# Kernel tuning notes

Measured on AMD Instinct MI355X. Metric: run time of the kernel, lower is better.

The kernel has to match this reference:

```python
import jax, jax.numpy as jnp
import numpy as np

B, T, D_IN, D, N = 8, 1024, 512, 512, 64

def setup_inputs() -> dict:
    key = jax.random.key(0)
    ks = jax.random.split(key, 8)
    s = 0.02  # weight init scale keeps tanh/softmax in sane range
    return {
        'x': jax.random.normal(ks[0], (B, T, D_IN), jnp.float32),
        'h_tape_init': jax.random.normal(ks[1], (B, N, D), jnp.float32),
        'h_work_init': jax.random.normal(ks[2], (B, D), jnp.float32) * 0.1,
        'W_h': jax.random.normal(ks[3], (D, D), jnp.float32) * s,
        'W_xz': jax.random.normal(ks[4], (2 * D, D_IN), jnp.float32) * s,
        'b_h': jnp.zeros((D,), jnp.float32),
        'W_write': jax.random.normal(ks[5], (D, D), jnp.float32) * s,
        'g_z': jnp.ones((D,), jnp.float32),
        'g_r': jnp.ones((D,), jnp.float32),
        'g_h': jnp.ones((D,), jnp.float32),
        'b_gate': jnp.zeros((D,), jnp.float32),
    }

def reference(x, h_tape_init, h_work_init, W_h, W_xz, b_h, W_write, g_z, g_r, g_h, b_gate):
    d = W_h.shape[0]
    scale = 1.0 / np.sqrt(d).astype(np.float32)
    xz = jnp.einsum('btk,ek->bte', x, W_xz)          # [B,T,2D]
    x_proj = xz[..., :d]
    z = xz[..., d:]

    def step(carry, inp):
        h_tape, h_work = carry                        # [B,N,D], [B,D]
        x_t, z_t = inp                                # [B,D], [B,D]
        read_scores = jnp.einsum('bd,bnd->bn', h_work, h_tape) * scale
        read_attn = jax.nn.softmax(read_scores, axis=-1)
        read_val = jnp.einsum('bn,bnd->bd', read_attn, h_tape)
        h_new = jnp.tanh(x_t + h_work @ W_h.T + read_val + b_h)
        write_val = h_new @ W_write.T
        write_scores = jnp.einsum('bd,bnd->bn', write_val, h_tape) * scale
        write_attn = jax.nn.softmax(write_scores, axis=-1)[..., None]  # [B,N,1]
        h_tape_new = h_tape * (1.0 - write_attn) + write_val[:, None, :] * write_attn
        gate_in = jnp.clip(z_t * g_z + read_val * g_r + h_new * g_h + b_gate, -20.0, 20.0)
        out = h_new * jax.nn.silu(gate_in)
        return (h_tape_new, h_new), out

    (h_tape_final, _), outs = jax.lax.scan(
        step, (h_tape_init, h_work_init),
        (jnp.swapaxes(x_proj, 0, 1), jnp.swapaxes(z, 0, 1)))
    return jnp.swapaxes(outs, 0, 1), h_tape_final
```

## Files before the change

### kernel.cpp

```cpp
#include <hip/hip_runtime.h>
#include <math.h>

#define BB 8
#define TT 1024
#define DD 512
#define NT 64
#define NSL 8
#define DSL 64
#define PITCH 68

static __device__ __forceinline__ float aload(const float* p) {
    return __hip_atomic_load(p, __ATOMIC_RELAXED, __HIP_MEMORY_SCOPE_AGENT);
}
static __device__ __forceinline__ void astore(float* p, float v) {
    __hip_atomic_store(p, v, __ATOMIC_RELAXED, __HIP_MEMORY_SCOPE_AGENT);
}

static __device__ __forceinline__ float redux8(float v) {
    v += __shfl_xor(v, 1);
    v += __shfl_xor(v, 2);
    v += __shfl_xor(v, 4);
    return v;
}

static __device__ __forceinline__ float softmax64(float sc) {
    float m = sc;
    #pragma unroll
    for (int off = 32; off > 0; off >>= 1) m = fmaxf(m, __shfl_xor(m, off));
    float e = __expf(sc - m);
    float s = e;
    #pragma unroll
    for (int off = 32; off > 0; off >>= 1) s += __shfl_xor(s, off);
    return e / s;
}

static __device__ __forceinline__ float dot64(const float4 (&w)[16], const float* hr) {
    float a0 = 0.f, a1 = 0.f, a2 = 0.f, a3 = 0.f;
    #pragma unroll
    for (int j = 0; j < 16; j += 4) {
        float4 h0 = *(const float4*)(hr + 4 * (j + 0));
        float4 h1 = *(const float4*)(hr + 4 * (j + 1));
        float4 h2 = *(const float4*)(hr + 4 * (j + 2));
        float4 h3 = *(const float4*)(hr + 4 * (j + 3));
        a0 += w[j + 0].x * h0.x + w[j + 0].y * h0.y + w[j + 0].z * h0.z + w[j + 0].w * h0.w;
        a1 += w[j + 1].x * h1.x + w[j + 1].y * h1.y + w[j + 1].z * h1.z + w[j + 1].w * h1.w;
        a2 += w[j + 2].x * h2.x + w[j + 2].y * h2.y + w[j + 2].z * h2.z + w[j + 2].w * h2.w;
        a3 += w[j + 3].x * h3.x + w[j + 3].y * h3.y + w[j + 3].z * h3.z + w[j + 3].w * h3.w;
    }
    return (a0 + a1) + (a2 + a3);
}

__global__ __launch_bounds__(256) void proj_kernel(const float* __restrict__ x,
                                                   const float* __restrict__ Wxz,
                                                   float* __restrict__ xp,
                                                   float* __restrict__ z) {
    __shared__ float As[16][66];
    __shared__ float Bs[16][66];
    const int m0 = blockIdx.x * 64;
    const int n0 = blockIdx.y * 64;
    const int tid = threadIdx.x;
    const int tm = tid / 16, tn = tid % 16;
    float c[4][4] = {};
    for (int k0 = 0; k0 < 512; k0 += 16) {
        const int r = tid >> 2, c4 = (tid & 3) * 4;
        float4 a4 = *(const float4*)(x + (size_t)(m0 + r) * 512 + k0 + c4);
        float4 b4 = *(const float4*)(Wxz + (size_t)(n0 + r) * 512 + k0 + c4);
        As[c4 + 0][r] = a4.x; As[c4 + 1][r] = a4.y; As[c4 + 2][r] = a4.z; As[c4 + 3][r] = a4.w;
        Bs[c4 + 0][r] = b4.x; Bs[c4 + 1][r] = b4.y; Bs[c4 + 2][r] = b4.z; Bs[c4 + 3][r] = b4.w;
        __syncthreads();
        #pragma unroll
        for (int k = 0; k < 16; ++k) {
            float a0 = As[k][tm * 4 + 0], a1 = As[k][tm * 4 + 1];
            float a2 = As[k][tm * 4 + 2], a3 = As[k][tm * 4 + 3];
            float b0 = Bs[k][tn * 4 + 0], b1 = Bs[k][tn * 4 + 1];
            float b2 = Bs[k][tn * 4 + 2], b3 = Bs[k][tn * 4 + 3];
            c[0][0] += a0 * b0; c[0][1] += a0 * b1; c[0][2] += a0 * b2; c[0][3] += a0 * b3;
            c[1][0] += a1 * b0; c[1][1] += a1 * b1; c[1][2] += a1 * b2; c[1][3] += a1 * b3;
            c[2][0] += a2 * b0; c[2][1] += a2 * b1; c[2][2] += a2 * b2; c[2][3] += a2 * b3;
            c[3][0] += a3 * b0; c[3][1] += a3 * b1; c[3][2] += a3 * b2; c[3][3] += a3 * b3;
        }
        __syncthreads();
    }
    #pragma unroll
    for (int i = 0; i < 4; ++i) {
        const int m = m0 + tm * 4 + i;
        #pragma unroll
        for (int j = 0; j < 4; ++j) {
            const int e = n0 + tn * 4 + j;
            if (e < 512) xp[(size_t)m * 512 + e] = c[i][j];
            else         z[(size_t)m * 512 + (e - 512)] = c[i][j];
        }
    }
}

__global__ __launch_bounds__(512, 2) void rec_kernel(
    const float* __restrict__ tape0, const float* __restrict__ hwork0,
    const float* __restrict__ W_h, const float* __restrict__ b_h,
    const float* __restrict__ W_write,
    const float* __restrict__ g_z, const float* __restrict__ g_r,
    const float* __restrict__ g_h, const float* __restrict__ b_gate,
    const float* __restrict__ Zbuf,
    float* __restrict__ out, float* __restrict__ tape_out,
    float* g_hn, float* g_pws, float* g_ps0, float* g_phwv,
    unsigned* flags) {
    const int b = blockIdx.x & 7;
    const int s = blockIdx.x >> 3;
    const int tid = threadIdx.x;
    const int row = tid >> 3;
    const int l = tid & 7;
    const int d0 = s * DSL;
    const int drow = d0 + row;
    const float scale = 0.044194173824159216f;

    __shared__ __attribute__((aligned(16))) float tape[NT][PITCH];
    __shared__ __attribute__((aligned(16))) float hw2[8][PITCH];
    __shared__ __attribute__((aligned(16))) float red[8][PITCH];
    __shared__ __attribute__((aligned(16))) float hn_s[DSL];
    __shared__ __attribute__((aligned(16))) float wv_s[DSL];
    __shared__ __attribute__((aligned(16))) float a_l[NT];
    __shared__ __attribute__((aligned(16))) float r_l[NT];
    __shared__ __attribute__((aligned(16))) float rv[DSL];
    __shared__ __attribute__((aligned(16))) float xp_s[DSL];
    __shared__ __attribute__((aligned(16))) float z_s[DSL];

    unsigned* flagA = flags + b * 128;
    unsigned* flagB = flags + b * 128 + 64;

    float4 wh[16], ww[16];
    {
        const float4* w1 = (const float4*)(W_h + (size_t)drow * DD + l * 64);
        const float4* w2 = (const float4*)(W_write + (size_t)drow * DD + l * 64);
        #pragma unroll
        for (int j = 0; j < 16; ++j) wh[j] = w1[j];
        #pragma unroll
        for (int j = 0; j < 16; ++j) ww[j] = w2[j];
    }
    const float bh_r = b_h[drow];
    const int de = (tid >= 64 && tid < 128) ? (tid - 64) : 0;
    const float gzr = g_z[d0 + de], grr = g_r[d0 + de], ghr = g_h[d0 + de], bgr = b_gate[d0 + de];

    {
        const float4* tsrc = (const float4*)(tape0 + ((size_t)(b * NT + row)) * DD + d0 + l * 8);
        float4 t0 = tsrc[0], t1 = tsrc[1];
        *(float4*)&tape[row][l * 8] = t0;
        *(float4*)&tape[row][l * 8 + 4] = t1;
    }
    if (tid < 128) {
        float4 h4 = *(const float4*)(hwork0 + (size_t)b * DD + tid * 4);
        const int e = tid * 4;
        *(float4*)&hw2[e >> 6][e & 63] = h4;
    }
    __syncthreads();

    {
        float acc = 0.f;
        #pragma unroll
        for (int i = 0; i < 8; ++i) {
            const int dl = l * 8 + i;
            const int e = d0 + dl;
            acc += hw2[e >> 6][e & 63] * tape[row][dl];
        }
        acc = redux8(acc);
        if (l == 0) astore(&g_ps0[(b * NSL + s) * NT + row], acc);
    }
    __syncthreads();
    if (tid == 0) {
        __builtin_amdgcn_s_waitcnt(0);
        __hip_atomic_fetch_add(flagB, 1u, __ATOMIC_RELAXED, __HIP_MEMORY_SCOPE_AGENT);
        while (__hip_atomic_load(flagB, __ATOMIC_RELAXED, __HIP_MEMORY_SCOPE_AGENT) < 8u) {}
    }
    __syncthreads();
    if (tid < 64) {
        float s0 = 0.f;
        #pragma unroll
        for (int ss = 0; ss < 8; ++ss) s0 += aload(&g_ps0[(b * NSL + ss) * NT + tid]);
        r_l[tid] = softmax64(s0 * scale);
    }
    __syncthreads();
    {
        const int nc = tid >> 6, d = tid & 63;
        float acc = 0.f;
        #pragma unroll
        for (int i = 0; i < 8; ++i) acc += r_l[nc * 8 + i] * tape[nc * 8 + i][d];
        red[nc][d] = acc;
    }
    __syncthreads();
    if (tid < 64) {
        float acc = 0.f;
        #pragma unroll
        for (int nc = 0; nc < 8; ++nc) acc += red[nc][tid];
        rv[tid] = acc;
    }
    if (tid >= 64 && tid < 128) {
        xp_s[tid - 64] = out[((size_t)(b * TT)) * DD + d0 + (tid - 64)];
    } else if (tid >= 128 && tid < 192) {
        z_s[tid - 128] = Zbuf[((size_t)(b * TT)) * DD + d0 + (tid - 128)];
    }
    __syncthreads();

    for (int t = 0; t < TT; ++t) {
        {
            float acc = dot64(wh, &hw2[l][0]);
            acc = redux8(acc);
            float hn = tanhf(acc + xp_s[row] + rv[row] + bh_r);
            if (l == 0) hn_s[row] = hn;
        }
        __syncthreads();
        if (tid < 64) {
            astore(&g_hn[b * DD + d0 + tid], hn_s[tid]);
        } else if (tid < 128) {
            const int d = tid - 64;
            const float h = hn_s[d];
            float g = z_s[d] * gzr + rv[d] * grr + h * ghr + bgr;
            g = fminf(fmaxf(g, -20.f), 20.f);
            const float sig = 1.f / (1.f + __expf(-g));
            out[((size_t)(b * TT + t)) * DD + d0 + d] = h * g * sig;
        }
        __syncthreads();
        if (tid == 0) {
            __builtin_amdgcn_s_waitcnt(0);
            __hip_atomic_fetch_add(flagA, 1u, __ATOMIC_RELAXED, __HIP_MEMORY_SCOPE_AGENT);
            const unsigned tgt = 8u * (unsigned)(t + 1);
            while (__hip_atomic_load(flagA, __ATOMIC_RELAXED, __HIP_MEMORY_SCOPE_AGENT) < tgt) {}
        }
        __syncthreads();
        if (tid < 128) {
            const int e = tid * 4;
            float v0 = aload(&g_hn[b * DD + e + 0]);
            float v1 = aload(&g_hn[b * DD + e + 1]);
            float v2 = aload(&g_hn[b * DD + e + 2]);
            float v3 = aload(&g_hn[b * DD + e + 3]);
            float4 h4; h4.x = v0; h4.y = v1; h4.z = v2; h4.w = v3;
            *(float4*)&hw2[e >> 6][e & 63] = h4;
        }
        __syncthreads();
        {
            float acc = dot64(ww, &hw2[l][0]);
            acc = redux8(acc);
            if (l == 0) wv_s[row] = acc;
        }
        __syncthreads();
        {
            float accw = 0.f, acc0 = 0.f;
            #pragma unroll
            for (int i = 0; i < 8; ++i) {
                const int dl = l * 8 + i;
                const float tp = tape[row][dl];
                accw += wv_s[dl] * tp;
                acc0 += hn_s[dl] * tp;
            }
            accw = redux8(accw);
            acc0 = redux8(acc0);
            if (l == 0) {
                astore(&g_pws[(b * NSL + s) * NT + row], accw);
                astore(&g_ps0[(b * NSL + s) * NT + row], acc0);
            }
        }
        if (tid < 8) {
            float a = 0.f;
            #pragma unroll
            for (int i = 0; i < 8; ++i) a += hn_s[tid * 8 + i] * wv_s[tid * 8 + i];
            a = redux8(a);
            if (tid == 0) astore(&g_phwv[b * NSL + s], a);
        }
        __syncthreads();
        if (tid == 0) {
            __builtin_amdgcn_s_waitcnt(0);
            __hip_atomic_fetch_add(flagB, 1u, __ATOMIC_RELAXED, __HIP_MEMORY_SCOPE_AGENT);
            const unsigned tgt = 8u * (unsigned)(t + 2);
            while (__hip_atomic_load(flagB, __ATOMIC_RELAXED, __HIP_MEMORY_SCOPE_AGENT) < tgt) {}
        } else if (tid >= 64 && tid < 128) {
            const int tn = (t + 1 < TT) ? (t + 1) : t;
            xp_s[tid - 64] = out[((size_t)(b * TT + tn)) * DD + d0 + (tid - 64)];
        } else if (tid >= 128 && tid < 192) {
            const int tn = (t + 1 < TT) ? (t + 1) : t;
            z_s[tid - 128] = Zbuf[((size_t)(b * TT + tn)) * DD + d0 + (tid - 128)];
        }
        __syncthreads();
        if (tid < 64) {
            float ws = 0.f, s0 = 0.f;
            #pragma unroll
            for (int ss = 0; ss < 8; ++ss) {
                ws += aload(&g_pws[(b * NSL + ss) * NT + tid]);
                s0 += aload(&g_ps0[(b * NSL + ss) * NT + tid]);
            }
            float hwv = 0.f;
            #pragma unroll
            for (int ss = 0; ss < 8; ++ss) hwv += aload(&g_phwv[b * NSL + ss]);
            const float a = softmax64(ws * scale);
            a_l[tid] = a;
            const float scn = scale * ((1.f - a) * s0 + a * hwv);
            r_l[tid] = softmax64(scn);
        }
        __syncthreads();
        {
            const float an = a_l[row];
            #pragma unroll
            for (int i = 0; i < 8; i += 4) {
                float4 tp = *(const float4*)&tape[row][l * 8 + i];
                float4 w4 = *(const float4*)&wv_s[l * 8 + i];
                tp.x += an * (w4.x - tp.x);
                tp.y += an * (w4.y - tp.y);
                tp.z += an * (w4.z - tp.z);
                tp.w += an * (w4.w - tp.w);
                *(float4*)&tape[row][l * 8 + i] = tp;
            }
        }
        __syncthreads();
        {
            const int nc = tid >> 6, d = tid & 63;
            float acc = 0.f;
            #pragma unroll
            for (int i = 0; i < 8; ++i) acc += r_l[nc * 8 + i] * tape[nc * 8 + i][d];
            red[nc][d] = acc;
        }
        __syncthreads();
        if (tid < 64) {
            float acc = 0.f;
            #pragma unroll
            for (int nc = 0; nc < 8; ++nc) acc += red[nc][tid];
            rv[tid] = acc;
        }
        __syncthreads();
    }

    {
        float4 t0 = *(const float4*)&tape[row][l * 8];
        float4 t1 = *(const float4*)&tape[row][l * 8 + 4];
        float* dst = tape_out + ((size_t)(b * NT + row)) * DD + d0 + l * 8;
        *(float4*)dst = t0;
        *(float4*)(dst + 4) = t1;
    }
}

extern "C" void kernel_launch(void* const* d_in, const int* in_sizes, int n_in,
                              void* d_out, int out_size, void* d_ws, size_t ws_size,
                              hipStream_t stream) {
    const float* x       = (const float*)d_in[0];
    const float* tape0   = (const float*)d_in[1];
    const float* hwork0  = (const float*)d_in[2];
    const float* W_h     = (const float*)d_in[3];
    const float* W_xz    = (const float*)d_in[4];
    const float* b_h     = (const float*)d_in[5];
    const float* W_write = (const float*)d_in[6];
    const float* g_z     = (const float*)d_in[7];
    const float* g_r     = (const float*)d_in[8];
    const float* g_h     = (const float*)d_in[9];
    const float* b_gate  = (const float*)d_in[10];

    float* out  = (float*)d_out;
    float* tout = out + (size_t)BB * TT * DD;

    char* ws = (char*)d_ws;
    unsigned* flags = (unsigned*)ws;
    float* g_hn   = (float*)(ws + 4096);
    float* g_pws  = (float*)(ws + 4096 + 16384);
    float* g_ps0  = (float*)(ws + 4096 + 32768);
    float* g_phwv = (float*)(ws + 4096 + 49152);
    float* Zbuf   = (float*)(ws + 65536);

    (void)in_sizes; (void)n_in; (void)out_size; (void)ws_size;

    hipMemsetAsync(flags, 0, 4096, stream);
    dim3 pgrid(128, 16);
    proj_kernel<<<pgrid, 256, 0, stream>>>(x, W_xz, out, Zbuf);
    rec_kernel<<<64, 512, 0, stream>>>(tape0, hwork0, W_h, b_h, W_write,
                                       g_z, g_r, g_h, b_gate, Zbuf,
                                       out, tout, g_hn, g_pws, g_ps0, g_phwv, flags);
}
```

Measured before the change: 5.949 ms.

## Replicate full tape per block and use tagged fp16 mailboxes for cross-block exchange

Each block now keeps the whole 64x512 tape of its batch in shared memory instead of a 64-column slice. Every block recomputes the full read and write scores locally, so the cross-block score reduction disappears. Per step, the only data exchanged between blocks are the new hidden state and partial W_write products, packed as fp16 pairs with a timestep tag in 64-bit atomics and double-buffered by parity. These replace the counter-flag barriers that ran twice per step. The cost is redundant tape work in every block, more shared memory, fp16 rounding of the exchanged hidden and write values, and a fast tanh approximation.

```diff
diff --git a/kernel.cpp b/kernel.cpp
--- a/kernel.cpp
+++ b/kernel.cpp
@@ -1,37 +1,41 @@
 #include <hip/hip_runtime.h>
 #include <math.h>
 
-#define BB 8
 #define TT 1024
 #define DD 512
-#define NT 64
-#define NSL 8
-#define DSL 64
-#define PITCH 68
-
-static __device__ __forceinline__ float aload(const float* p) {
+#define PITCH 516
+
+typedef unsigned int u32;
+typedef unsigned long long u64;
+typedef _Float16 half2_t __attribute__((ext_vector_type(2)));
+
+static __device__ __forceinline__ u64 aload64(const u64* p) {
     return __hip_atomic_load(p, __ATOMIC_RELAXED, __HIP_MEMORY_SCOPE_AGENT);
 }
-static __device__ __forceinline__ void astore(float* p, float v) {
+static __device__ __forceinline__ void astore64(u64* p, u64 v) {
     __hip_atomic_store(p, v, __ATOMIC_RELAXED, __HIP_MEMORY_SCOPE_AGENT);
 }
+static __device__ __forceinline__ u32 pkh2(float lo, float hi) {
+    return __builtin_bit_cast(u32, __builtin_amdgcn_cvt_pkrtz(lo, hi));
+}
+static __device__ __forceinline__ float2 uph2(u32 v) {
+    half2_t h = __builtin_bit_cast(half2_t, v);
+    return make_float2((float)h.x, (float)h.y);
+}
 
 static __device__ __forceinline__ float redux8(float v) {
-    v += __shfl_xor(v, 1);
-    v += __shfl_xor(v, 2);
-    v += __shfl_xor(v, 4);
+    v += __shfl_xor(v, 1); v += __shfl_xor(v, 2); v += __shfl_xor(v, 4); return v;
+}
+static __device__ __forceinline__ float sum64(float v) {
+    #pragma unroll
+    for (int o = 32; o > 0; o >>= 1) v += __shfl_xor(v, o);
     return v;
 }
-
-static __device__ __forceinline__ float softmax64(float sc) {
-    float m = sc;
-    #pragma unroll
-    for (int off = 32; off > 0; off >>= 1) m = fmaxf(m, __shfl_xor(m, off));
-    float e = __expf(sc - m);
-    float s = e;
-    #pragma unroll
-    for (int off = 32; off > 0; off >>= 1) s += __shfl_xor(s, off);
-    return e / s;
+static __device__ __forceinline__ float expc(float x) { return __expf(fminf(x, 60.f)); }
+static __device__ __forceinline__ float fast_tanh(float x) {
+    float xc = fminf(fmaxf(x, -15.f), 15.f);
+    float e = __expf(2.f * xc);
+    return (e - 1.f) / (e + 1.f);
 }
 
 static __device__ __forceinline__ float dot64(const float4 (&w)[16], const float* hr) {
@@ -93,7 +97,7 @@
     }
 }
 
-__global__ __launch_bounds__(512, 2) void rec_kernel(
+__global__ __launch_bounds__(512) void rec_kernel(
     const float* __restrict__ tape0, const float* __restrict__ hwork0,
     const float* __restrict__ W_h, const float* __restrict__ b_h,
     const float* __restrict__ W_write,
@@ -101,235 +105,248 @@
     const float* __restrict__ g_h, const float* __restrict__ b_gate,
     const float* __restrict__ Zbuf,
     float* __restrict__ out, float* __restrict__ tape_out,
-    float* g_hn, float* g_pws, float* g_ps0, float* g_phwv,
-    unsigned* flags) {
-    const int b = blockIdx.x & 7;
-    const int s = blockIdx.x >> 3;
-    const int tid = threadIdx.x;
-    const int row = tid >> 3;
-    const int l = tid & 7;
-    const int d0 = s * DSL;
-    const int drow = d0 + row;
+    u64* hbuf, u64* cbuf) {
+    extern __shared__ float smem[];
+    float* tape = smem;
+    float* hf   = smem + 64 * PITCH;
+    float* wvs  = hf + 512;
+    float* rvc  = wvs + 512;
+    float* hn_s = rvc + 512;
+    float* hh_s = hn_s + 64;
+    float* ws_s = hh_s + 64;
+    float* q0_s = ws_s + 64;
+    float2* ac_s = (float2*)(q0_s + 64);
+    float* xpc  = (float*)(ac_s + 64);
+    float* zc   = xpc + 64;
+    float* misc = zc + 64;
+
+    const int b = blockIdx.x & 7, s = blockIdx.x >> 3;
+    const int tid = threadIdx.x, lane = tid & 63, wid = tid >> 6;
+    const int r8 = tid >> 3, l = tid & 7;
+    const int d0 = s * 64;
     const float scale = 0.044194173824159216f;
 
-    __shared__ __attribute__((aligned(16))) float tape[NT][PITCH];
-    __shared__ __attribute__((aligned(16))) float hw2[8][PITCH];
-    __shared__ __attribute__((aligned(16))) float red[8][PITCH];
-    __shared__ __attribute__((aligned(16))) float hn_s[DSL];
-    __shared__ __attribute__((aligned(16))) float wv_s[DSL];
-    __shared__ __attribute__((aligned(16))) float a_l[NT];
-    __shared__ __attribute__((aligned(16))) float r_l[NT];
-    __shared__ __attribute__((aligned(16))) float rv[DSL];
-    __shared__ __attribute__((aligned(16))) float xp_s[DSL];
-    __shared__ __attribute__((aligned(16))) float z_s[DSL];
-
-    unsigned* flagA = flags + b * 128;
-    unsigned* flagB = flags + b * 128 + 64;
-
-    float4 wh[16], ww[16];
+    float4 wh[16];
+    float4 wwc[16];
     {
-        const float4* w1 = (const float4*)(W_h + (size_t)drow * DD + l * 64);
-        const float4* w2 = (const float4*)(W_write + (size_t)drow * DD + l * 64);
+        const float4* w1 = (const float4*)(W_h + (size_t)(d0 + r8) * DD + l * 64);
         #pragma unroll
         for (int j = 0; j < 16; ++j) wh[j] = w1[j];
+        const float4* w2 = (const float4*)(W_write + (size_t)tid * DD + d0);
         #pragma unroll
-        for (int j = 0; j < 16; ++j) ww[j] = w2[j];
-    }
-    const float bh_r = b_h[drow];
-    const int de = (tid >= 64 && tid < 128) ? (tid - 64) : 0;
-    const float gzr = g_z[d0 + de], grr = g_r[d0 + de], ghr = g_h[d0 + de], bgr = b_gate[d0 + de];
+        for (int j = 0; j < 16; ++j) wwc[j] = w2[j];
+    }
+    float gz = 0.f, gr = 0.f, gh = 0.f, bg = 0.f, bhr = 0.f;
+    if (wid == 0) bhr = b_h[d0 + lane];
+    if (wid == 1) { gz = g_z[d0 + lane]; gr = g_r[d0 + lane]; gh = g_h[d0 + lane]; bg = b_gate[d0 + lane]; }
+
+    #pragma unroll
+    for (int rr = 0; rr < 8; ++rr) {
+        const int n = 8 * wid + rr;
+        const float4* src = (const float4*)(tape0 + ((size_t)(b * 64 + n)) * DD);
+        float4 t0 = src[lane * 2], t1 = src[lane * 2 + 1];
+        *(float4*)(tape + n * PITCH + lane * 8) = t0;
+        *(float4*)(tape + n * PITCH + lane * 8 + 4) = t1;
+    }
+
+    for (int t = 0; t < TT; ++t) {
+        float xpr = 0.f, zr = 0.f;
+        if (wid == 2)      xpr = out[((size_t)(b * TT + t)) * DD + d0 + lane];
+        else if (wid == 3) zr  = Zbuf[((size_t)(b * TT + t)) * DD + d0 + lane];
+
+        if (t == 0) {
+            if (tid < 128) ((float4*)hf)[tid] = ((const float4*)(hwork0 + (size_t)b * DD))[tid];
+            wvs[tid] = 0.f;
+        } else {
+            const int par = t & 1;
+            const u32 tg = (u32)t;
+            if (tid < 256) {
+                const u64* base = cbuf + ((size_t)(par * 8 + b) * 8) * 256 + tid;
+                u64 v[8];
+                for (;;) {
+                    bool ok = true;
+                    #pragma unroll
+                    for (int j = 0; j < 8; ++j) v[j] = aload64(base + j * 256);
+                    #pragma unroll
+                    for (int j = 0; j < 8; ++j) ok = ok && ((u32)(v[j] >> 32) == tg);
+                    if (ok) break;
+                    __builtin_amdgcn_s_sleep(2);
+                }
+                float a0 = 0.f, a1 = 0.f;
+                #pragma unroll
+                for (int j = 0; j < 8; ++j) { float2 p = uph2((u32)v[j]); a0 += p.x; a1 += p.y; }
+                wvs[2 * tid] = a0; wvs[2 * tid + 1] = a1;
+            } else {
+                const int k = tid - 256;
+                const u64* p = hbuf + (size_t)(par * 8 + b) * 256 + k;
+                u64 v;
+                for (;;) {
+                    v = aload64(p);
+                    if ((u32)(v >> 32) == tg) break;
+                    __builtin_amdgcn_s_sleep(2);
+                }
+                float2 hp = uph2((u32)v);
+                hf[2 * k] = hp.x; hf[2 * k + 1] = hp.y;
+            }
+        }
+        __syncthreads();
+
+        {
+            float acc = dot64(wh, hf + l * 64);
+            acc = redux8(acc);
+            if (l == 0) hh_s[r8] = acc;
+        }
+        if (wid == 0) {
+            float q = 0.f;
+            #pragma unroll
+            for (int i = 0; i < 8; ++i) q += hf[lane * 8 + i] * wvs[lane * 8 + i];
+            q = sum64(q);
+            if (lane == 0) misc[0] = q;
+        }
+        {
+            float4 wa = ((const float4*)wvs)[lane * 2], wb = ((const float4*)wvs)[lane * 2 + 1];
+            float4 ha = ((const float4*)hf)[lane * 2],  hb2 = ((const float4*)hf)[lane * 2 + 1];
+            #pragma unroll
+            for (int rr = 0; rr < 8; ++rr) {
+                const int n = 8 * wid + rr;
+                const float4 t0 = *(const float4*)(tape + n * PITCH + lane * 8);
+                const float4 t1 = *(const float4*)(tape + n * PITCH + lane * 8 + 4);
+                float pw = t0.x * wa.x + t0.y * wa.y + t0.z * wa.z + t0.w * wa.w
+                         + t1.x * wb.x + t1.y * wb.y + t1.z * wb.z + t1.w * wb.w;
+                float pq = t0.x * ha.x + t0.y * ha.y + t0.z * ha.z + t0.w * ha.w
+                         + t1.x * hb2.x + t1.y * hb2.y + t1.z * hb2.z + t1.w * hb2.w;
+                pw = sum64(pw); pq = sum64(pq);
+                if (lane == 0) { ws_s[n] = pw; q0_s[n] = pq; }
+            }
+        }
+        __syncthreads();
+
+        if (wid == 0) {
+            float a = 0.f;
+            if (t > 0) {
+                float ew = expc(scale * ws_s[lane]);
+                float Zw = sum64(ew);
+                a = __fdividef(ew, Zw);
+            }
+            float sc = scale * ((1.f - a) * q0_s[lane] + a * misc[0]);
+            float er = expc(sc);
+            float Zr = sum64(er);
+            float r_ = __fdividef(er, Zr);
+            ac_s[lane] = make_float2(a, r_ * (1.f - a));
+            float c2 = sum64(r_ * a);
+            if (lane == 0) misc[1] = c2;
+        } else if (wid == 2) xpc[lane] = xpr;
+        else if (wid == 3)   zc[lane] = zr;
+        __syncthreads();
+
+        {
+            const int d = tid;
+            const float wvd = wvs[d];
+            const float c2 = misc[1];
+            float acc = 0.f;
+            #pragma unroll 8
+            for (int n = 0; n < 64; ++n) {
+                float2 ac = ac_s[n];
+                float tp = tape[n * PITCH + d];
+                acc += ac.y * tp;
+                tape[n * PITCH + d] = tp + ac.x * (wvd - tp);
+            }
+            rvc[d] = acc + c2 * wvd;
+        }
+        __syncthreads();
+
+        if (wid == 0) hn_s[lane] = fast_tanh(xpc[lane] + hh_s[lane] + rvc[d0 + lane] + bhr);
+        __syncthreads();
+
+        {
+            float cj = 0.f;
+            #pragma unroll
+            for (int j = 0; j < 16; ++j) {
+                float4 h4 = ((const float4*)hn_s)[j];
+                cj += wwc[j].x * h4.x + wwc[j].y * h4.y + wwc[j].z * h4.z + wwc[j].w * h4.w;
+            }
+            float cn = __shfl_xor(cj, 1);
+            const int par2 = (t + 1) & 1;
+            const u32 tg = (u32)(t + 1);
+            if ((tid & 1) == 0)
+                astore64(cbuf + (((size_t)(par2 * 8 + b) * 8) + s) * 256 + (tid >> 1),
+                         ((u64)tg << 32) | (u64)pkh2(cj, cn));
+            if (tid < 32)
+                astore64(hbuf + (size_t)(par2 * 8 + b) * 256 + s * 32 + tid,
+                         ((u64)tg << 32) | (u64)pkh2(hn_s[2 * tid], hn_s[2 * tid + 1]));
+            if (wid == 1) {
+                float h = hn_s[lane];
+                float g = zc[lane] * gz + rvc[d0 + lane] * gr + h * gh + bg;
+                g = fminf(fmaxf(g, -20.f), 20.f);
+                float sig = 1.f / (1.f + __expf(-g));
+                out[((size_t)(b * TT + t)) * DD + d0 + lane] = h * g * sig;
+            }
+        }
+    }
 
     {
-        const float4* tsrc = (const float4*)(tape0 + ((size_t)(b * NT + row)) * DD + d0 + l * 8);
-        float4 t0 = tsrc[0], t1 = tsrc[1];
-        *(float4*)&tape[row][l * 8] = t0;
-        *(float4*)&tape[row][l * 8 + 4] = t1;
-    }
-    if (tid < 128) {
-        float4 h4 = *(const float4*)(hwork0 + (size_t)b * DD + tid * 4);
-        const int e = tid * 4;
-        *(float4*)&hw2[e >> 6][e & 63] = h4;
-    }
-    __syncthreads();
-
-    {
-        float acc = 0.f;
-        #pragma unroll
-        for (int i = 0; i < 8; ++i) {
-            const int dl = l * 8 + i;
-            const int e = d0 + dl;
-            acc += hw2[e >> 6][e & 63] * tape[row][dl];
-        }
-        acc = redux8(acc);
-        if (l == 0) astore(&g_ps0[(b * NSL + s) * NT + row], acc);
-    }
-    __syncthreads();
-    if (tid == 0) {
-        __builtin_amdgcn_s_waitcnt(0);
-        __hip_atomic_fetch_add(flagB, 1u, __ATOMIC_RELAXED, __HIP_MEMORY_SCOPE_AGENT);
-        while (__hip_atomic_load(flagB, __ATOMIC_RELAXED, __HIP_MEMORY_SCOPE_AGENT) < 8u) {}
-    }
-    __syncthreads();
-    if (tid < 64) {
-        float s0 = 0.f;
-        #pragma unroll
-        for (int ss = 0; ss < 8; ++ss) s0 += aload(&g_ps0[(b * NSL + ss) * NT + tid]);
-        r_l[tid] = softmax64(s0 * scale);
-    }
-    __syncthreads();
-    {
-        const int nc = tid >> 6, d = tid & 63;
-        float acc = 0.f;
-        #pragma unroll
-        for (int i = 0; i < 8; ++i) acc += r_l[nc * 8 + i] * tape[nc * 8 + i][d];
-        red[nc][d] = acc;
-    }
-    __syncthreads();
-    if (tid < 64) {
-        float acc = 0.f;
-        #pragma unroll
-        for (int nc = 0; nc < 8; ++nc) acc += red[nc][tid];
-        rv[tid] = acc;
-    }
-    if (tid >= 64 && tid < 128) {
-        xp_s[tid - 64] = out[((size_t)(b * TT)) * DD + d0 + (tid - 64)];
-    } else if (tid >= 128 && tid < 192) {
-        z_s[tid - 128] = Zbuf[((size_t)(b * TT)) * DD + d0 + (tid - 128)];
-    }
-    __syncthreads();
-
-    for (int t = 0; t < TT; ++t) {
-        {
-            float acc = dot64(wh, &hw2[l][0]);
-            acc = redux8(acc);
-            float hn = tanhf(acc + xp_s[row] + rv[row] + bh_r);
-            if (l == 0) hn_s[row] = hn;
-        }
-        __syncthreads();
-        if (tid < 64) {
-            astore(&g_hn[b * DD + d0 + tid], hn_s[tid]);
-        } else if (tid < 128) {
-            const int d = tid - 64;
-            const float h = hn_s[d];
-            float g = z_s[d] * gzr + rv[d] * grr + h * ghr + bgr;
-            g = fminf(fmaxf(g, -20.f), 20.f);
-            const float sig = 1.f / (1.f + __expf(-g));
-            out[((size_t)(b * TT + t)) * DD + d0 + d] = h * g * sig;
-        }
-        __syncthreads();
-        if (tid == 0) {
-            __builtin_amdgcn_s_waitcnt(0);
-            __hip_atomic_fetch_add(flagA, 1u, __ATOMIC_RELAXED, __HIP_MEMORY_SCOPE_AGENT);
-            const unsigned tgt = 8u * (unsigned)(t + 1);
-            while (__hip_atomic_load(flagA, __ATOMIC_RELAXED, __HIP_MEMORY_SCOPE_AGENT) < tgt) {}
-        }
-        __syncthreads();
-        if (tid < 128) {
-            const int e = tid * 4;
-            float v0 = aload(&g_hn[b * DD + e + 0]);
-            float v1 = aload(&g_hn[b * DD + e + 1]);
-            float v2 = aload(&g_hn[b * DD + e + 2]);
-            float v3 = aload(&g_hn[b * DD + e + 3]);
-            float4 h4; h4.x = v0; h4.y = v1; h4.z = v2; h4.w = v3;
-            *(float4*)&hw2[e >> 6][e & 63] = h4;
-        }
-        __syncthreads();
-        {
-            float acc = dot64(ww, &hw2[l][0]);
-            acc = redux8(acc);
-            if (l == 0) wv_s[row] = acc;
-        }
-        __syncthreads();
-        {
-            float accw = 0.f, acc0 = 0.f;
-            #pragma unroll
-            for (int i = 0; i < 8; ++i) {
-                const int dl = l * 8 + i;
-                const float tp = tape[row][dl];
-                accw += wv_s[dl] * tp;
-                acc0 += hn_s[dl] * tp;
-            }
-            accw = redux8(accw);
-            acc0 = redux8(acc0);
-            if (l == 0) {
-                astore(&g_pws[(b * NSL + s) * NT + row], accw);
-                astore(&g_ps0[(b * NSL + s) * NT + row], acc0);
-            }
-        }
-        if (tid < 8) {
-            float a = 0.f;
-            #pragma unroll
-            for (int i = 0; i < 8; ++i) a += hn_s[tid * 8 + i] * wv_s[tid * 8 + i];
-            a = redux8(a);
-            if (tid == 0) astore(&g_phwv[b * NSL + s], a);
-        }
-        __syncthreads();
-        if (tid == 0) {
-            __builtin_amdgcn_s_waitcnt(0);
-            __hip_atomic_fetch_add(flagB, 1u, __ATOMIC_RELAXED, __HIP_MEMORY_SCOPE_AGENT);
-            const unsigned tgt = 8u * (unsigned)(t + 2);
-            while (__hip_atomic_load(flagB, __ATOMIC_RELAXED, __HIP_MEMORY_SCOPE_AGENT) < tgt) {}
-        } else if (tid >= 64 && tid < 128) {
-            const int tn = (t + 1 < TT) ? (t + 1) : t;
-            xp_s[tid - 64] = out[((size_t)(b * TT + tn)) * DD + d0 + (tid - 64)];
-        } else if (tid >= 128 && tid < 192) {
-            const int tn = (t + 1 < TT) ? (t + 1) : t;
-            z_s[tid - 128] = Zbuf[((size_t)(b * TT + tn)) * DD + d0 + (tid - 128)];
-        }
-        __syncthreads();
-        if (tid < 64) {
-            float ws = 0.f, s0 = 0.f;
-            #pragma unroll
-            for (int ss = 0; ss < 8; ++ss) {
-                ws += aload(&g_pws[(b * NSL + ss) * NT + tid]);
-                s0 += aload(&g_ps0[(b * NSL + ss) * NT + tid]);
-            }
-            float hwv = 0.f;
-            #pragma unroll
-            for (int ss = 0; ss < 8; ++ss) hwv += aload(&g_phwv[b * NSL + ss]);
-            const float a = softmax64(ws * scale);
-            a_l[tid] = a;
-            const float scn = scale * ((1.f - a) * s0 + a * hwv);
-            r_l[tid] = softmax64(scn);
-        }
-        __syncthreads();
-        {
-            const float an = a_l[row];
-            #pragma unroll
-            for (int i = 0; i < 8; i += 4) {
-                float4 tp = *(const float4*)&tape[row][l * 8 + i];
-                float4 w4 = *(const float4*)&wv_s[l * 8 + i];
-                tp.x += an * (w4.x - tp.x);
-                tp.y += an * (w4.y - tp.y);
-                tp.z += an * (w4.z - tp.z);
-                tp.w += an * (w4.w - tp.w);
-                *(float4*)&tape[row][l * 8 + i] = tp;
-            }
-        }
-        __syncthreads();
-        {
-            const int nc = tid >> 6, d = tid & 63;
-            float acc = 0.f;
-            #pragma unroll
-            for (int i = 0; i < 8; ++i) acc += r_l[nc * 8 + i] * tape[nc * 8 + i][d];
-            red[nc][d] = acc;
-        }
-        __syncthreads();
-        if (tid < 64) {
-            float acc = 0.f;
-            #pragma unroll
-            for (int nc = 0; nc < 8; ++nc) acc += red[nc][tid];
-            rv[tid] = acc;
-        }
-        __syncthreads();
-    }
-
-    {
-        float4 t0 = *(const float4*)&tape[row][l * 8];
-        float4 t1 = *(const float4*)&tape[row][l * 8 + 4];
-        float* dst = tape_out + ((size_t)(b * NT + row)) * DD + d0 + l * 8;
-        *(float4*)dst = t0;
-        *(float4*)(dst + 4) = t1;
+        const int par = TT & 1;
+        const u32 tg = (u32)TT;
+        if (tid < 256) {
+            const u64* base = cbuf + ((size_t)(par * 8 + b) * 8) * 256 + tid;
+            u64 v[8];
+            for (;;) {
+                bool ok = true;
+                #pragma unroll
+                for (int j = 0; j < 8; ++j) v[j] = aload64(base + j * 256);
+                #pragma unroll
+                for (int j = 0; j < 8; ++j) ok = ok && ((u32)(v[j] >> 32) == tg);
+                if (ok) break;
+                __builtin_amdgcn_s_sleep(2);
+            }
+            float a0 = 0.f, a1 = 0.f;
+            #pragma unroll
+            for (int j = 0; j < 8; ++j) { float2 p = uph2((u32)v[j]); a0 += p.x; a1 += p.y; }
+            wvs[2 * tid] = a0; wvs[2 * tid + 1] = a1;
+        }
+        __syncthreads();
+        {
+            float4 wa = ((const float4*)wvs)[lane * 2], wb = ((const float4*)wvs)[lane * 2 + 1];
+            #pragma unroll
+            for (int rr = 0; rr < 8; ++rr) {
+                const int n = 8 * wid + rr;
+                const float4 t0 = *(const float4*)(tape + n * PITCH + lane * 8);
+                const float4 t1 = *(const float4*)(tape + n * PITCH + lane * 8 + 4);
+                float pw = t0.x * wa.x + t0.y * wa.y + t0.z * wa.z + t0.w * wa.w
+                         + t1.x * wb.x + t1.y * wb.y + t1.z * wb.z + t1.w * wb.w;
+                pw = sum64(pw);
+                if (lane == 0) ws_s[n] = pw;
+            }
+        }
+        __syncthreads();
+        if (wid == 0) {
+            float ew = expc(scale * ws_s[lane]);
+            float Zw = sum64(ew);
+            ac_s[lane] = make_float2(__fdividef(ew, Zw), 0.f);
+        }
+        __syncthreads();
+        {
+            const int d = tid;
+            const float wvd = wvs[d];
+            #pragma unroll 8
+            for (int n = 0; n < 64; ++n) {
+                float2 ac = ac_s[n];
+                float tp = tape[n * PITCH + d];
+                tape[n * PITCH + d] = tp + ac.x * (wvd - tp);
+            }
+        }
+        __syncthreads();
+        if (s == 0) {
+            #pragma unroll
+            for (int rr = 0; rr < 8; ++rr) {
+                const int n = 8 * wid + rr;
+                float4 t0 = *(const float4*)(tape + n * PITCH + lane * 8);
+                float4 t1 = *(const float4*)(tape + n * PITCH + lane * 8 + 4);
+                float4* dst = (float4*)(tape_out + ((size_t)(b * 64 + n)) * DD);
+                dst[lane * 2] = t0;
+                dst[lane * 2 + 1] = t1;
+            }
+        }
     }
 }
 
@@ -349,22 +366,22 @@
     const float* b_gate  = (const float*)d_in[10];
 
     float* out  = (float*)d_out;
-    float* tout = out + (size_t)BB * TT * DD;
+    float* tout = out + (size_t)8 * TT * DD;
 
     char* ws = (char*)d_ws;
-    unsigned* flags = (unsigned*)ws;
-    float* g_hn   = (float*)(ws + 4096);
-    float* g_pws  = (float*)(ws + 4096 + 16384);
-    float* g_ps0  = (float*)(ws + 4096 + 32768);
-    float* g_phwv = (float*)(ws + 4096 + 49152);
-    float* Zbuf   = (float*)(ws + 65536);
+    u64* hbuf  = (u64*)ws;
+    u64* cbuf  = (u64*)(ws + 32768);
+    float* Zbuf = (float*)(ws + 327680);
 
     (void)in_sizes; (void)n_in; (void)out_size; (void)ws_size;
 
-    hipMemsetAsync(flags, 0, 4096, stream);
+    const int smem_bytes = (64 * PITCH + 3 * 512 + 4 * 64 + 128 + 2 * 64 + 4) * 4;
+    hipFuncSetAttribute((const void*)rec_kernel,
+                        hipFuncAttributeMaxDynamicSharedMemorySize, smem_bytes);
+
     dim3 pgrid(128, 16);
     proj_kernel<<<pgrid, 256, 0, stream>>>(x, W_xz, out, Zbuf);
-    rec_kernel<<<64, 512, 0, stream>>>(tape0, hwork0, W_h, b_h, W_write,
-                                       g_z, g_r, g_h, b_gate, Zbuf,
-                                       out, tout, g_hn, g_pws, g_ps0, g_phwv, flags);
-}
+    rec_kernel<<<64, 512, smem_bytes, stream>>>(tape0, hwork0, W_h, b_h, W_write,
+                                                g_z, g_r, g_h, b_gate, Zbuf,
+                                                out, tout, hbuf, cbuf);
+}
```

Measured after the change: 10.36 ms. 74.1% more time.
